# Kernel tuning notes

Hardware: AMD Instinct MI355X
Metric: run time of the kernel (lower is better)

## Reference

```python
import jax, jax.numpy as jnp
import numpy as np

H = 16          # tree height (bits); n = 2**H
TP = 8          # parallel coordinate copies
N = 2 ** H
K = 2 * H // 4  # k = f*h//division_fact = 8
C = 2 * K * H + 1   # 257 connection candidates
T, S = 128, 128


def setup_inputs() -> dict:
    key = jax.random.key(0)
    k1, k2, k3, k4 = jax.random.split(key, 4)
    # critbit integer coordinates in [1-n, n)
    sta_loc = jax.random.randint(k1, (T, TP), 1 - N, N, dtype=jnp.int32)
    pos_loc = jax.random.randint(k2, (T, S, TP), 1 - N, N, dtype=jnp.int32)
    cnc_loc = jax.random.randint(k3, (T, C, TP), 1 - N, N, dtype=jnp.int32)
    eu_norm = jax.random.uniform(k4, (T, S), dtype=jnp.float32)
    return {"sta_loc": sta_loc, "pos_loc": pos_loc, "cnc_loc": cnc_loc, "eu_norm": eu_norm}


def _distance(c1, c2, norm):
    # sign product: (+1 if >=0 else -1) for each coordinate
    sg = ((c1 >= 0).astype(jnp.float32) * 2.0 - 1.0) * ((c2 >= 0).astype(jnp.float32) * 2.0 - 1.0)
    xor = jnp.abs(c1) ^ jnp.abs(c2)
    # frexp exponent of (xor+1): e = floor(log2(xor+1)) + 1, same as torch.frexp
    _, e = jnp.frexp((xor + 1).astype(jnp.float32))
    s = e.astype(jnp.float32) / H
    return sg * (1.0 - s) * norm


def reference(sta_loc, pos_loc, cnc_loc, eu_norm):
    # (T,S,TP): distance of each anchor row to its sampled positives
    cos_sta_pos = _distance(sta_loc[:, None, :], pos_loc, eu_norm[..., None])
    cos_sta_pos_sum = cos_sta_pos.sum(axis=-1)                       # (T,S)
    # (T,S,C,TP): distance of every connection candidate to every positive
    cos_cnc_pos = _distance(cnc_loc[:, None, :, :], pos_loc[:, :, None, :],
                            eu_norm[..., None, None])
    # leave-one-coordinate-out substitution, averaged over TP copies
    ct_val = (cos_sta_pos_sum[:, :, None, None]
              - cos_sta_pos[:, :, None, :]
              + cos_cnc_pos) / TP                                    # (T,S,C,TP)
    return ct_val
```

## Files before the change

kernel.cpp:

```cpp
#include <hip/hip_runtime.h>


namespace {
constexpr int kTP = 8;
constexpr int kC  = 257;
constexpr int kT  = 128;
constexpr int kS  = 128;

typedef __attribute__((ext_vector_type(4))) int   int4v;
typedef __attribute__((ext_vector_type(4))) float float4v;

__device__ __forceinline__ float dist_f(int c1, int c2, float norm) {
    int x = (abs(c1) ^ abs(c2)) + 1;
    float f = (float)(__clz(x) - 16);
    float v = f * norm * (1.0f / 16.0f);
    return ((c1 ^ c2) < 0) ? -v : v;
}
}

__global__ __launch_bounds__(256) void critigraph_kernel(
    const int*   __restrict__ sta,
    const int*   __restrict__ pos,
    const int*   __restrict__ cnc,
    const float* __restrict__ eu,
    float*       __restrict__ out)
{
    __shared__ float s_csp[kTP];
    __shared__ float s_np8[kTP];
    __shared__ int   s_apos[kTP];

    const int bid = blockIdx.x;
    const int t = bid >> 7;
    const int s = bid & (kS - 1);
    const int tid = threadIdx.x;

    if (tid < kTP) {
        const int p  = tid;
        const int st = sta[t * kTP + p];
        const int po = pos[(t * kS + s) * kTP + p];
        const float norm = eu[t * kS + s];
        s_csp[p]  = dist_f(st, po, norm);
        s_apos[p] = abs(po);
        s_np8[p]  = (po >= 0 ? norm : -norm) * (1.0f / 128.0f);
    }
    __syncthreads();

    float csp[kTP], np8[kTP], base8[kTP];
    int   apos[kTP];
    float sum = 0.0f;
#pragma unroll
    for (int p = 0; p < kTP; ++p) {
        csp[p]  = s_csp[p];
        np8[p]  = s_np8[p];
        apos[p] = s_apos[p];
        sum += csp[p];
    }
#pragma unroll
    for (int p = 0; p < kTP; ++p)
        base8[p] = (sum - csp[p]) * 0.125f;

    const int* cbase = cnc + (size_t)t * kC * kTP;
    float* obase = out + (size_t)(t * kS + s) * (kC * kTP);

    for (int c = tid; c < kC; c += 256) {
        const int4v* cp = (const int4v*)(cbase + c * kTP);
        const int4v lo = cp[0];
        const int4v hi = cp[1];

        float4v r0, r1;
#pragma unroll
        for (int p = 0; p < kTP; ++p) {
            const int cn = (p < 4) ? lo[p] : hi[p - 4];
            const int x  = (abs(cn) ^ apos[p]) + 1;
            const float f = (float)(__clz(x) - 16);
            const float coeff = __int_as_float(
                __float_as_int(np8[p]) ^ (((unsigned)cn) & 0x80000000u));
            const float v = fmaf(f, coeff, base8[p]);
            if (p < 4) r0[p] = v; else r1[p - 4] = v;
        }

        float4v* op = (float4v*)(obase + c * kTP);
        op[0] = r0;
        op[1] = r1;
    }
}

extern "C" void kernel_launch(void* const* d_in, const int* in_sizes, int n_in,
                              void* d_out, int out_size, void* d_ws, size_t ws_size,
                              hipStream_t stream) {
    const int*   sta = (const int*)d_in[0];
    const int*   pos = (const int*)d_in[1];
    const int*   cnc = (const int*)d_in[2];
    const float* eu  = (const float*)d_in[3];
    float*       out = (float*)d_out;

    const dim3 grid(kT * kS);
    const dim3 block(256);
    critigraph_kernel<<<grid, block, 0, stream>>>(sta, pos, cnc, eu, out);
}
```

Baseline: 155.6 us.

## Process eight positives per block, reusing candidate loads and fixing tail handling

Each block now handles eight consecutive positive samples for one anchor instead of one, which cuts the grid by a factor of eight. Each thread loads its connection candidate row once and reuses it across the eight samples, and per-sample constants are staged in shared memory. The 257th candidate, which previously caused a second loop pass with mostly idle threads, is now handled separately by eight threads. The trade-off is fewer blocks, so less parallelism to hide store latency, in exchange for less redundant global loads and setup work.

```diff
diff --git a/kernel.cpp b/kernel.cpp
--- a/kernel.cpp
+++ b/kernel.cpp
@@ -2,20 +2,15 @@
 
 
 namespace {
-constexpr int kTP = 8;
-constexpr int kC  = 257;
-constexpr int kT  = 128;
-constexpr int kS  = 128;
+constexpr int kTP   = 8;
+constexpr int kC    = 257;
+constexpr int kT    = 128;
+constexpr int kS    = 128;
+constexpr int kSB   = 8;
+constexpr int kTile = kS / kSB;
 
 typedef __attribute__((ext_vector_type(4))) int   int4v;
 typedef __attribute__((ext_vector_type(4))) float float4v;
-
-__device__ __forceinline__ float dist_f(int c1, int c2, float norm) {
-    int x = (abs(c1) ^ abs(c2)) + 1;
-    float f = (float)(__clz(x) - 16);
-    float v = f * norm * (1.0f / 16.0f);
-    return ((c1 ^ c2) < 0) ? -v : v;
-}
 }
 
 __global__ __launch_bounds__(256) void critigraph_kernel(
@@ -25,63 +20,98 @@
     const float* __restrict__ eu,
     float*       __restrict__ out)
 {
-    __shared__ float s_csp[kTP];
-    __shared__ float s_np8[kTP];
-    __shared__ int   s_apos[kTP];
+    __shared__ int   s_apos[kSB][kTP];
+    __shared__ float s_np8[kSB][kTP];
+    __shared__ float s_csp[kSB][kTP];
+    __shared__ float s_base8[kSB][kTP];
 
-    const int bid = blockIdx.x;
-    const int t = bid >> 7;
-    const int s = bid & (kS - 1);
+    const int t   = blockIdx.x >> 4;
+    const int s0  = (blockIdx.x & (kTile - 1)) * kSB;
     const int tid = threadIdx.x;
+
+    if (tid < kSB * kTP) {
+        const int sl = tid >> 3;
+        const int p  = tid & 7;
+        const int s  = s0 + sl;
+        const int st = sta[t * kTP + p];
+        const int po = pos[(t * kS + s) * kTP + p];
+        const float norm = eu[t * kS + s];
+        const int x = (abs(st) ^ abs(po)) + 1;
+        const float f = (float)(__clz(x) - 16);
+        const float v = f * norm * (1.0f / 16.0f);
+        s_csp[sl][p]  = ((st ^ po) < 0) ? -v : v;
+        s_apos[sl][p] = abs(po);
+        s_np8[sl][p]  = (po >= 0 ? norm : -norm) * (1.0f / 128.0f);
+    }
+    __syncthreads();
+    if (tid < kSB * kTP) {
+        const int sl = tid >> 3;
+        const int p  = tid & 7;
+        float sum = 0.0f;
+#pragma unroll
+        for (int q = 0; q < kTP; ++q) sum += s_csp[sl][q];
+        s_base8[sl][p] = (sum - s_csp[sl][p]) * 0.125f;
+    }
+    __syncthreads();
+
+    {
+        const int c = tid;
+        const int* cb = cnc + ((size_t)t * kC + c) * kTP;
+        const int4v lo = *(const int4v*)cb;
+        const int4v hi = *(const int4v*)(cb + 4);
+        int      acn[kTP];
+        unsigned sg[kTP];
+#pragma unroll
+        for (int p = 0; p < kTP; ++p) {
+            const int cn = (p < 4) ? lo[p] : hi[p - 4];
+            acn[p] = abs(cn);
+            sg[p]  = ((unsigned)cn) & 0x80000000u;
+        }
+
+        float* ob = out + ((size_t)(t * kS + s0) * kC + c) * kTP;
+#pragma unroll
+        for (int sl = 0; sl < kSB; ++sl) {
+            const int4v   ap0 = *(const int4v*)&s_apos[sl][0];
+            const int4v   ap1 = *(const int4v*)&s_apos[sl][4];
+            const float4v np0 = *(const float4v*)&s_np8[sl][0];
+            const float4v np1 = *(const float4v*)&s_np8[sl][4];
+            const float4v b0  = *(const float4v*)&s_base8[sl][0];
+            const float4v b1  = *(const float4v*)&s_base8[sl][4];
+
+            float4v r0, r1;
+#pragma unroll
+            for (int p = 0; p < 4; ++p) {
+                const int x = (acn[p] ^ ap0[p]) + 1;
+                const float f = (float)(__clz(x) - 16);
+                const float coeff = __int_as_float(__float_as_int(np0[p]) ^ sg[p]);
+                r0[p] = fmaf(f, coeff, b0[p]);
+            }
+#pragma unroll
+            for (int p = 0; p < 4; ++p) {
+                const int x = (acn[p + 4] ^ ap1[p]) + 1;
+                const float f = (float)(__clz(x) - 16);
+                const float coeff = __int_as_float(__float_as_int(np1[p]) ^ sg[p + 4]);
+                r1[p] = fmaf(f, coeff, b1[p]);
+            }
+            *(float4v*)ob       = r0;
+            *(float4v*)(ob + 4) = r1;
+            ob += (size_t)kC * kTP;
+        }
+    }
 
     if (tid < kTP) {
         const int p  = tid;
-        const int st = sta[t * kTP + p];
-        const int po = pos[(t * kS + s) * kTP + p];
-        const float norm = eu[t * kS + s];
-        s_csp[p]  = dist_f(st, po, norm);
-        s_apos[p] = abs(po);
-        s_np8[p]  = (po >= 0 ? norm : -norm) * (1.0f / 128.0f);
-    }
-    __syncthreads();
-
-    float csp[kTP], np8[kTP], base8[kTP];
-    int   apos[kTP];
-    float sum = 0.0f;
+        const int cn = cnc[((size_t)t * kC + (kC - 1)) * kTP + p];
+        const int a  = abs(cn);
+        const unsigned sg = ((unsigned)cn) & 0x80000000u;
+        float* ob = out + ((size_t)(t * kS + s0) * kC + (kC - 1)) * kTP + p;
 #pragma unroll
-    for (int p = 0; p < kTP; ++p) {
-        csp[p]  = s_csp[p];
-        np8[p]  = s_np8[p];
-        apos[p] = s_apos[p];
-        sum += csp[p];
-    }
-#pragma unroll
-    for (int p = 0; p < kTP; ++p)
-        base8[p] = (sum - csp[p]) * 0.125f;
-
-    const int* cbase = cnc + (size_t)t * kC * kTP;
-    float* obase = out + (size_t)(t * kS + s) * (kC * kTP);
-
-    for (int c = tid; c < kC; c += 256) {
-        const int4v* cp = (const int4v*)(cbase + c * kTP);
-        const int4v lo = cp[0];
-        const int4v hi = cp[1];
-
-        float4v r0, r1;
-#pragma unroll
-        for (int p = 0; p < kTP; ++p) {
-            const int cn = (p < 4) ? lo[p] : hi[p - 4];
-            const int x  = (abs(cn) ^ apos[p]) + 1;
+        for (int sl = 0; sl < kSB; ++sl) {
+            const int x = (a ^ s_apos[sl][p]) + 1;
             const float f = (float)(__clz(x) - 16);
-            const float coeff = __int_as_float(
-                __float_as_int(np8[p]) ^ (((unsigned)cn) & 0x80000000u));
-            const float v = fmaf(f, coeff, base8[p]);
-            if (p < 4) r0[p] = v; else r1[p - 4] = v;
+            const float coeff = __int_as_float(__float_as_int(s_np8[sl][p]) ^ sg);
+            ob[(size_t)sl * kC * kTP] = fmaf(f, coeff, s_base8[sl][p]);
         }
-
-        float4v* op = (float4v*)(obase + c * kTP);
-        op[0] = r0;
-        op[1] = r1;
     }
 }
 
@@ -94,7 +124,7 @@
     const float* eu  = (const float*)d_in[3];
     float*       out = (float*)d_out;
 
-    const dim3 grid(kT * kS);
+    const dim3 grid(kT * kTile);
     const dim3 block(256);
     critigraph_kernel<<<grid, block, 0, stream>>>(sta, pos, cnc, eu, out);
 }
```

New measurement: 147.8 us. 1.05x faster.
